# Performance work log

Hardware: AMD Instinct MI355X
Metric: run time of the kernel (lower is better)

Reference implementation:

```python
import jax, jax.numpy as jnp
import numpy as np

T, I, H = 32768, 512, 512

def setup_inputs() -> dict:
    key = jax.random.key(0)
    k1, k2, k3, k4, k5 = jax.random.split(key, 5)
    lim = 1.0 / np.sqrt(H)
    xs = jax.random.normal(k1, (T, I), dtype=jnp.float32)
    weight_ih = jax.random.uniform(k2, (3 * H, I), minval=-lim, maxval=lim, dtype=jnp.float32)
    weight_hh = jax.random.uniform(k3, (3 * H, H), minval=-lim, maxval=lim, dtype=jnp.float32)
    bias = jax.random.uniform(k4, (3 * H,), minval=-lim, maxval=lim, dtype=jnp.float32)
    bias_n = jax.random.uniform(k5, (H,), minval=-lim, maxval=lim, dtype=jnp.float32)
    return {"xs": xs, "weight_ih": weight_ih, "weight_hh": weight_hh, "bias": bias, "bias_n": bias_n}

def reference(xs, weight_ih, weight_hh, bias, bias_n):
    hidden_size = weight_hh.shape[1]
    # Input-side gate projections for all timesteps in one GEMM (math-identical
    # to equinox GRUCell's per-step weight_ih @ x + bias).
    igates_all = xs @ weight_ih.T + bias  # (T, 3H)

    def step(h, ig):
        ir, iz, in_ = jnp.split(ig, 3)
        hr, hz, hn = jnp.split(weight_hh @ h, 3)
        r = jax.nn.sigmoid(ir + hr)          # reset gate
        z = jax.nn.sigmoid(iz + hz)          # update ("input") gate
        n = jnp.tanh(in_ + r * (hn + bias_n))  # candidate
        h_new = n + z * (h - n)
        return h_new, h_new

    h0 = jnp.zeros(hidden_size, dtype=xs.dtype)
    _, outs = jax.lax.scan(step, h0, igates_all)
    return outs
```

## Files before the change

### kernel.cpp

```cpp
#include <hip/hip_runtime.h>


#define T_STEPS 32768
#define HID     512
#define NBLK    32
#define HS      16
#define RING    4
#define SPIN_CAP (1u << 18)

#define FMA4(acc, W, g, vv)                                                   \
    acc = fmaf(W[g][(kk << 2) + 0], vv.x, acc);                               \
    acc = fmaf(W[g][(kk << 2) + 1], vv.y, acc);                               \
    acc = fmaf(W[g][(kk << 2) + 2], vv.z, acc);                               \
    acc = fmaf(W[g][(kk << 2) + 3], vv.w, acc);

__global__ __launch_bounds__(256, 1) void gru_persistent(
    const float* __restrict__ xs,
    const float* __restrict__ w_ih,
    const float* __restrict__ w_hh,
    const float* __restrict__ bias,
    const float* __restrict__ bias_n,
    float* __restrict__ out,
    unsigned long long* __restrict__ hbuf)
{
    const int b    = blockIdx.x;
    const int tid  = threadIdx.x;
    const int wave = tid >> 6;
    const int lane = tid & 63;
    const int jl   = (wave << 2) + (lane >> 4);
    const int sub  = lane & 15;
    const int j    = b * HS + jl;
    const int c0   = sub << 5;

    __shared__ float x_s[2][HID];
    __shared__ float h_s[HID];

    float wih[3][32], whh[3][32];
#pragma unroll
    for (int g = 0; g < 3; ++g) {
        const float* rih = w_ih + (size_t)(g * HID + j) * HID + c0;
        const float* rhh = w_hh + (size_t)(g * HID + j) * HID + c0;
#pragma unroll
        for (int kk = 0; kk < 8; ++kk) {
            const int c = ((sub + kk) & 7) << 2;
            const float4 a  = *(const float4*)(rih + c);
            const float4 bb = *(const float4*)(rhh + c);
            wih[g][(kk << 2) + 0] = a.x;  wih[g][(kk << 2) + 1] = a.y;
            wih[g][(kk << 2) + 2] = a.z;  wih[g][(kk << 2) + 3] = a.w;
            whh[g][(kk << 2) + 0] = bb.x; whh[g][(kk << 2) + 1] = bb.y;
            whh[g][(kk << 2) + 2] = bb.z; whh[g][(kk << 2) + 3] = bb.w;
        }
    }
    const float b_r  = bias[j];
    const float b_z  = bias[HID + j];
    const float b_nn = bias[2 * HID + j];
    const float bn2  = bias_n[j];

    const int xi = tid << 1;
    float2 xreg = *(const float2*)(xs + xi);
    x_s[0][xi] = xreg.x; x_s[0][xi + 1] = xreg.y;
    xreg = *(const float2*)(xs + HID + xi);
    __syncthreads();

    float hprev = 0.f;
    bool  dead  = false;

    for (int t = 0; t < T_STEPS; ++t) {
        float ar = 0.f, az = 0.f, an = 0.f;
        const float* xb = x_s[t & 1];
#pragma unroll
        for (int kk = 0; kk < 8; ++kk) {
            const int c = c0 + (((sub + kk) & 7) << 2);
            const float4 xv = *(const float4*)(xb + c);
            FMA4(ar, wih, 0, xv)
            FMA4(az, wih, 1, xv)
            FMA4(an, wih, 2, xv)
        }

        if (t > 0) {
            const unsigned long long* src =
                hbuf + ((size_t)((t - 1) & (RING - 1)) * HID) + xi;
            const unsigned int tag = (unsigned int)t;
            unsigned long long v0 = 0, v1 = 0;
            if (!dead) {
                unsigned int it = 0;
                do {
                    v0 = __hip_atomic_load(src, __ATOMIC_RELAXED,
                                           __HIP_MEMORY_SCOPE_AGENT);
                } while ((unsigned int)(v0 >> 32) != tag && ++it < SPIN_CAP);
                if (it >= SPIN_CAP) dead = true;
                it = 0;
                do {
                    v1 = __hip_atomic_load(src + 1, __ATOMIC_RELAXED,
                                           __HIP_MEMORY_SCOPE_AGENT);
                } while ((unsigned int)(v1 >> 32) != tag && ++it < SPIN_CAP);
                if (it >= SPIN_CAP) dead = true;
            }
            h_s[xi]     = __uint_as_float((unsigned int)v0);
            h_s[xi + 1] = __uint_as_float((unsigned int)v1);
        } else {
            h_s[xi] = 0.f; h_s[xi + 1] = 0.f;
        }
        __syncthreads();

        float hr = 0.f, hz = 0.f, hn = 0.f;
#pragma unroll
        for (int kk = 0; kk < 8; ++kk) {
            const int c = c0 + (((sub + kk) & 7) << 2);
            const float4 hv = *(const float4*)(h_s + c);
            FMA4(hr, whh, 0, hv)
            FMA4(hz, whh, 1, hv)
            FMA4(hn, whh, 2, hv)
        }

        float s1 = ar + hr, s2 = az + hz, s3 = an, s4 = hn;
#pragma unroll
        for (int m = 1; m < 16; m <<= 1) {
            s1 += __shfl_xor(s1, m);
            s2 += __shfl_xor(s2, m);
            s3 += __shfl_xor(s3, m);
            s4 += __shfl_xor(s4, m);
        }

        if (sub == 0) {
            const float r = 1.f / (1.f + __expf(-(s1 + b_r)));
            const float z = 1.f / (1.f + __expf(-(s2 + b_z)));
            const float n = tanhf(s3 + b_nn + r * (s4 + bn2));
            const float h = n + z * (hprev - n);
            hprev = h;
            out[(size_t)t * HID + j] = h;
            const unsigned long long pv =
                ((unsigned long long)(unsigned int)(t + 1) << 32) |
                (unsigned long long)__float_as_uint(h);
            __hip_atomic_store(hbuf + ((size_t)(t & (RING - 1)) * HID) + j, pv,
                               __ATOMIC_RELAXED, __HIP_MEMORY_SCOPE_AGENT);
        }

        x_s[(t + 1) & 1][xi]     = xreg.x;
        x_s[(t + 1) & 1][xi + 1] = xreg.y;
        {
            const int tn = (t + 2 < T_STEPS) ? (t + 2) : (T_STEPS - 1);
            xreg = *(const float2*)(xs + (size_t)tn * HID + xi);
        }
        __syncthreads();
    }
}

extern "C" void kernel_launch(void* const* d_in, const int* in_sizes, int n_in,
                              void* d_out, int out_size, void* d_ws, size_t ws_size,
                              hipStream_t stream) {
    const float* xs     = (const float*)d_in[0];
    const float* w_ih   = (const float*)d_in[1];
    const float* w_hh   = (const float*)d_in[2];
    const float* bias   = (const float*)d_in[3];
    const float* bias_n = (const float*)d_in[4];
    float* out = (float*)d_out;
    unsigned long long* hbuf = (unsigned long long*)d_ws;

    hipMemsetAsync(d_ws, 0, (size_t)RING * HID * sizeof(unsigned long long), stream);

    hipLaunchKernelGGL(gru_persistent, dim3(NBLK), dim3(256), 0, stream,
                       xs, w_ih, w_hh, bias, bias_n, out, hbuf);
}
```

Baseline: 81.65 ms.

## Issue speculative vectorized h poll before input GEMV and streamline gate math

Each step now issues one uncached 128-bit load for both tagged hidden values before the input-projection FMAs, so the cross-block latency overlaps compute. It falls back to a combined spin only if the tags are stale. Per-step state exchange becomes a single dwordx4 instead of two serialized atomic 64-bit loads. Gate math switches to fast sigmoid and tanh, computed on all lanes, and the hbuf store now comes before the output store. A periodic __syncthreads_or lets the kernel exit on timeout, which adds a small reduction cost every 16 steps and relies on inline asm for cache bypass and wait counts.

After: 86.60 ms. +6.1%, slower.

```diff
diff --git a/kernel.cpp b/kernel.cpp
--- a/kernel.cpp
+++ b/kernel.cpp
@@ -6,7 +6,20 @@
 #define NBLK    32
 #define HS      16
 #define RING    4
-#define SPIN_CAP (1u << 18)
+#define POLL_CAP (1u << 17)
+
+typedef unsigned int       u32;
+typedef unsigned long long u64;
+typedef u32 u32x4 __attribute__((ext_vector_type(4)));
+
+__device__ __forceinline__ float fast_sig(float x) {
+    return __fdividef(1.f, 1.f + __expf(-x));
+}
+__device__ __forceinline__ float fast_tanh(float x) {
+    x = fminf(15.f, fmaxf(-15.f, x));
+    const float e = __expf(2.f * x);
+    return __fdividef(e - 1.f, e + 1.f);
+}
 
 #define FMA4(acc, W, g, vv)                                                   \
     acc = fmaf(W[g][(kk << 2) + 0], vv.x, acc);                               \
@@ -21,7 +34,7 @@
     const float* __restrict__ bias,
     const float* __restrict__ bias_n,
     float* __restrict__ out,
-    unsigned long long* __restrict__ hbuf)
+    u64* __restrict__ hbuf)
 {
     const int b    = blockIdx.x;
     const int tid  = threadIdx.x;
@@ -64,53 +77,60 @@
 
     float hprev = 0.f;
     bool  dead  = false;
+    u32x4 hv;
 
     for (int t = 0; t < T_STEPS; ++t) {
+        const u64* src = hbuf + ((size_t)((t - 1) & (RING - 1)) * HID) + xi;
+        if (t > 0) {
+            asm volatile("global_load_dwordx4 %0, %1, off sc0 sc1"
+                         : "=v"(hv) : "v"(src) : "memory");
+        }
+
         float ar = 0.f, az = 0.f, an = 0.f;
-        const float* xb = x_s[t & 1];
+        {
+            const float* xb = x_s[t & 1];
 #pragma unroll
-        for (int kk = 0; kk < 8; ++kk) {
-            const int c = c0 + (((sub + kk) & 7) << 2);
-            const float4 xv = *(const float4*)(xb + c);
-            FMA4(ar, wih, 0, xv)
-            FMA4(az, wih, 1, xv)
-            FMA4(an, wih, 2, xv)
+            for (int kk = 0; kk < 8; ++kk) {
+                const int c = c0 + (((sub + kk) & 7) << 2);
+                const float4 xv = *(const float4*)(xb + c);
+                FMA4(ar, wih, 0, xv)
+                FMA4(az, wih, 1, xv)
+                FMA4(an, wih, 2, xv)
+            }
         }
 
         if (t > 0) {
-            const unsigned long long* src =
-                hbuf + ((size_t)((t - 1) & (RING - 1)) * HID) + xi;
-            const unsigned int tag = (unsigned int)t;
-            unsigned long long v0 = 0, v1 = 0;
-            if (!dead) {
-                unsigned int it = 0;
+            const u32 tag = (u32)t;
+            asm volatile("s_waitcnt vmcnt(0)" : "+v"(hv) :: "memory");
+            if (!dead && (hv.y != tag || hv.w != tag)) {
+                u32 it = 0;
                 do {
-                    v0 = __hip_atomic_load(src, __ATOMIC_RELAXED,
-                                           __HIP_MEMORY_SCOPE_AGENT);
-                } while ((unsigned int)(v0 >> 32) != tag && ++it < SPIN_CAP);
-                if (it >= SPIN_CAP) dead = true;
-                it = 0;
-                do {
-                    v1 = __hip_atomic_load(src + 1, __ATOMIC_RELAXED,
-                                           __HIP_MEMORY_SCOPE_AGENT);
-                } while ((unsigned int)(v1 >> 32) != tag && ++it < SPIN_CAP);
-                if (it >= SPIN_CAP) dead = true;
+                    asm volatile("global_load_dwordx4 %0, %1, off sc0 sc1\n\t"
+                                 "s_waitcnt vmcnt(0)"
+                                 : "=v"(hv) : "v"(src) : "memory");
+                } while ((hv.y != tag || hv.w != tag) && ++it < POLL_CAP);
+                if (it >= POLL_CAP) dead = true;
             }
-            h_s[xi]     = __uint_as_float((unsigned int)v0);
-            h_s[xi + 1] = __uint_as_float((unsigned int)v1);
+            h_s[xi]     = __uint_as_float(hv.x);
+            h_s[xi + 1] = __uint_as_float(hv.z);
         } else {
             h_s[xi] = 0.f; h_s[xi + 1] = 0.f;
         }
-        __syncthreads();
+
+        if ((t & 15) == 0) {
+            if (__syncthreads_or((int)dead)) break;
+        } else {
+            __syncthreads();
+        }
 
         float hr = 0.f, hz = 0.f, hn = 0.f;
 #pragma unroll
         for (int kk = 0; kk < 8; ++kk) {
             const int c = c0 + (((sub + kk) & 7) << 2);
-            const float4 hv = *(const float4*)(h_s + c);
-            FMA4(hr, whh, 0, hv)
-            FMA4(hz, whh, 1, hv)
-            FMA4(hn, whh, 2, hv)
+            const float4 hv4 = *(const float4*)(h_s + c);
+            FMA4(hr, whh, 0, hv4)
+            FMA4(hz, whh, 1, hv4)
+            FMA4(hn, whh, 2, hv4)
         }
 
         float s1 = ar + hr, s2 = az + hz, s3 = an, s4 = hn;
@@ -122,18 +142,16 @@
             s4 += __shfl_xor(s4, m);
         }
 
+        const float r = fast_sig(s1 + b_r);
+        const float z = fast_sig(s2 + b_z);
+        const float n = fast_tanh(s3 + b_nn + r * (s4 + bn2));
+        const float h = n + z * (hprev - n);
+        hprev = h;
         if (sub == 0) {
-            const float r = 1.f / (1.f + __expf(-(s1 + b_r)));
-            const float z = 1.f / (1.f + __expf(-(s2 + b_z)));
-            const float n = tanhf(s3 + b_nn + r * (s4 + bn2));
-            const float h = n + z * (hprev - n);
-            hprev = h;
-            out[(size_t)t * HID + j] = h;
-            const unsigned long long pv =
-                ((unsigned long long)(unsigned int)(t + 1) << 32) |
-                (unsigned long long)__float_as_uint(h);
+            const u64 pv = ((u64)(u32)(t + 1) << 32) | (u64)__float_as_uint(h);
             __hip_atomic_store(hbuf + ((size_t)(t & (RING - 1)) * HID) + j, pv,
                                __ATOMIC_RELAXED, __HIP_MEMORY_SCOPE_AGENT);
+            out[(size_t)t * HID + j] = h;
         }
 
         x_s[(t + 1) & 1][xi]     = xreg.x;
@@ -155,9 +173,9 @@
     const float* bias   = (const float*)d_in[3];
     const float* bias_n = (const float*)d_in[4];
     float* out = (float*)d_out;
-    unsigned long long* hbuf = (unsigned long long*)d_ws;
+    u64* hbuf = (u64*)d_ws;
 
-    hipMemsetAsync(d_ws, 0, (size_t)RING * HID * sizeof(unsigned long long), stream);
+    hipMemsetAsync(d_ws, 0, (size_t)RING * HID * sizeof(u64), stream);
 
     hipLaunchKernelGGL(gru_persistent, dim3(NBLK), dim3(256), 0, stream,
                        xs, w_ih, w_hh, bias, bias_n, out, hbuf);
```
